# Kernel tuning notes

Measured on AMD Instinct MI355X. Metric: run time of the kernel, lower is better.

## Reference

```python
import jax, jax.numpy as jnp
import numpy as np

N = 100000
E = 1600000
C_IN = 128
C_OUT = 128
BN_EPS = 1e-5


def setup_inputs() -> dict:
    key = jax.random.key(0)
    k1, k2, k3, k4 = jax.random.split(key, 4)
    x = jax.random.normal(k1, (N, C_IN), dtype=jnp.float32)
    edge_index = jax.random.randint(k2, (2, E), 0, N, dtype=jnp.int64)
    edge_weight = jax.random.uniform(k3, (E,), dtype=jnp.float32)
    W = jax.random.normal(k4, (C_IN, C_OUT), dtype=jnp.float32) / np.sqrt(C_IN)
    gamma = jnp.ones((C_OUT,), dtype=jnp.float32)
    beta = jnp.zeros((C_OUT,), dtype=jnp.float32)
    return {"x": x, "edge_index": edge_index, "edge_weight": edge_weight,
            "W": W, "gamma": gamma, "beta": beta}


def reference(x, edge_index, edge_weight, W, gamma, beta):
    n = x.shape[0]
    row, col = edge_index[0], edge_index[1]  # messages flow row -> col
    loop = jnp.arange(n, dtype=edge_index.dtype)
    # GCNConv (improved=False): add self-loops with weight 1
    row_f = jnp.concatenate([row, loop])
    col_f = jnp.concatenate([col, loop])
    w_f = jnp.concatenate([edge_weight, jnp.ones((n,), x.dtype)])
    # symmetric normalization: D^{-1/2} A D^{-1/2}
    deg = jax.ops.segment_sum(w_f, col_f, num_segments=n)
    deg_safe = jnp.where(deg > 0, deg, 1.0)
    dis = jnp.where(deg > 0, jax.lax.rsqrt(deg_safe), 0.0)
    norm = dis[row_f] * w_f * dis[col_f]  # [E+N]
    # linear transform then scatter-add aggregation (bias=False)
    h = x @ W  # [N, C_out]
    agg = jax.ops.segment_sum(h[row_f] * norm[:, None], col_f, num_segments=n)
    # BatchNorm1d (training mode: batch stats, biased variance) + ReLU
    mean = agg.mean(axis=0)
    var = agg.var(axis=0)
    y = (agg - mean) * jax.lax.rsqrt(var + BN_EPS) * gamma + beta
    return jax.nn.relu(y)
```

## Files before the change

kernel.cpp:

```cpp
#include <hip/hip_runtime.h>

#define C 128
#define MAXNB 1024
typedef unsigned int uint;
typedef unsigned short ushort;
typedef __attribute__((ext_vector_type(4))) float f32x4;
typedef __attribute__((ext_vector_type(8))) short bf16x8;

__device__ __forceinline__ float blo(uint u) { return __uint_as_float(u << 16); }
__device__ __forceinline__ float bhi(uint u) { return __uint_as_float(u & 0xFFFF0000u); }
#define PACKBF(LO, HI) __builtin_amdgcn_perm(__float_as_uint(HI) + 0x8000u, \
                                             __float_as_uint(LO) + 0x8000u, 0x07060302u)

__global__ __launch_bounds__(256) void k_hist(const int* __restrict__ col,
                                              int* __restrict__ counts,
                                              int nE, int NB, int NBLK) {
    __shared__ int hist[MAXNB];
    const int t = threadIdx.x, blk = blockIdx.x;
    for (int i = t; i < NB; i += 256) hist[i] = 0;
    __syncthreads();
    const int base = blk * 2048;
    for (int k = 0; k < 8; ++k) {
        int e = base + k * 256 + t;
        if (e < nE) atomicAdd(&hist[col[e] >> 7], 1);
    }
    __syncthreads();
    for (int i = t; i < NB; i += 256) counts[i * NBLK + blk] = hist[i];
}

__global__ __launch_bounds__(256) void k_scan1(int* __restrict__ counts,
                                               int* __restrict__ bsum, int scanN) {
    __shared__ int s[256];
    int t = threadIdx.x;
    int i = blockIdx.x * 256 + t;
    int v = (i < scanN) ? counts[i] : 0;
    s[t] = v;
    __syncthreads();
    for (int d = 1; d < 256; d <<= 1) {
        int a = (t >= d) ? s[t - d] : 0;
        __syncthreads();
        s[t] += a;
        __syncthreads();
    }
    if (i < scanN) counts[i] = s[t] - v;
    if (t == 255) bsum[blockIdx.x] = s[255];
}

__global__ __launch_bounds__(256) void k_scan2(int* __restrict__ bsum, int nb) {
    __shared__ int s[256];
    __shared__ int carry;
    int t = threadIdx.x;
    if (t == 0) carry = 0;
    __syncthreads();
    int nch = (nb + 255) / 256;
    for (int c = 0; c < nch; ++c) {
        int i = c * 256 + t;
        int v = (i < nb) ? bsum[i] : 0;
        s[t] = v;
        __syncthreads();
        for (int d = 1; d < 256; d <<= 1) {
            int a = (t >= d) ? s[t - d] : 0;
            __syncthreads();
            s[t] += a;
            __syncthreads();
        }
        int cb = carry;
        if (i < nb) bsum[i] = s[t] - v + cb;
        int tot = s[255];
        __syncthreads();
        if (t == 0) carry = cb + tot;
        __syncthreads();
    }
}

__global__ __launch_bounds__(256) void k_scan3(int* __restrict__ counts,
                                               const int* __restrict__ bsum,
                                               int* __restrict__ bstart,
                                               int scanN, int NBLK, int NB, int nE) {
    int i = blockIdx.x * 256 + threadIdx.x;
    if (i >= scanN) return;
    int v = counts[i] + bsum[i >> 8];
    counts[i] = v;
    if (i % NBLK == 0) {
        bstart[i / NBLK] = v;
        if (i == 0) bstart[NB] = nE;
    }
}

__global__ __launch_bounds__(256) void k_scatter(const int* __restrict__ ei,
                                                 const float* __restrict__ ew,
                                                 const int* __restrict__ counts,
                                                 int2* __restrict__ ev2,
                                                 int nE, int NB, int NBLK) {
    __shared__ int base_l[MAXNB];
    __shared__ int cnt_l[MAXNB];
    const int t = threadIdx.x, blk = blockIdx.x;
    for (int i = t; i < NB; i += 256) {
        base_l[i] = counts[i * NBLK + blk];
        cnt_l[i] = 0;
    }
    __syncthreads();
    const int base = blk * 2048;
    for (int k = 0; k < 8; ++k) {
        int e = base + k * 256 + t;
        if (e >= nE) continue;
        int c = ei[nE + e];
        int row = ei[e];
        int b = c >> 7;
        int pos = base_l[b] + atomicAdd(&cnt_l[b], 1);
        ev2[pos] = make_int2(((c & 127) << 25) | row, __float_as_int(ew[e]));
    }
}

__global__ __launch_bounds__(256) void k_sortdeg(const int2* __restrict__ ev2,
                                                 const int* __restrict__ bstart,
                                                 int2* __restrict__ evs,
                                                 int* __restrict__ offs,
                                                 float* __restrict__ dis,
                                                 int n, int nE) {
    __shared__ int cnt[128];
    __shared__ float wsum[128];
    __shared__ int cur[128];
    __shared__ int sc[128];
    const int t = threadIdx.x, b = blockIdx.x;
    if (t < 128) { cnt[t] = 0; wsum[t] = 0.f; }
    __syncthreads();
    const int s = bstart[b], e = bstart[b + 1];
    for (int i = s + t; i < e; i += 256) {
        int2 E = ev2[i];
        int cl = (uint)E.x >> 25;
        atomicAdd(&cnt[cl], 1);
        atomicAdd(&wsum[cl], __int_as_float(E.y));
    }
    __syncthreads();
    if (t < 128) sc[t] = cnt[t];
    __syncthreads();
    for (int d = 1; d < 128; d <<= 1) {
        int v = 0;
        if (t < 128 && t >= d) v = sc[t - d];
        __syncthreads();
        if (t < 128) sc[t] += v;
        __syncthreads();
    }
    if (t < 128) {
        int col = (b << 7) + t;
        int base = s + sc[t] - cnt[t];
        cur[t] = base;
        if (col < n) {
            offs[col] = base;
            dis[col] = rsqrtf(1.0f + wsum[t]);
        }
    }
    if (b == 0 && t == 0) offs[n] = nE;
    __syncthreads();
    for (int i = s + t; i < e; i += 256) {
        int2 E = ev2[i];
        int cl = (uint)E.x >> 25;
        int pos = atomicAdd(&cur[cl], 1);
        evs[pos] = make_int2(E.x & 0x1FFFFFF, E.y);
    }
}

__global__ __launch_bounds__(256) void k_cvt(const float4* __restrict__ x4,
                                             const float* __restrict__ dis,
                                             ushort4* __restrict__ xb4, long total4) {
    long i = (long)blockIdx.x * 256 + threadIdx.x;
    if (i >= total4) return;
    float d = dis[i >> 5];
    float4 v = x4[i];
    ushort4 r;
#define RNE(OUT, F)                                                     \
    {                                                                   \
        uint u = __float_as_uint((F) * d);                              \
        OUT = (ushort)((u + 0x7FFFu + ((u >> 16) & 1u)) >> 16);         \
    }
    RNE(r.x, v.x) RNE(r.y, v.y) RNE(r.z, v.z) RNE(r.w, v.w)
#undef RNE
    xb4[i] = r;
}

__global__ __launch_bounds__(256) void k_wcvt(const float* __restrict__ W,
                                              ushort* __restrict__ WbT) {
    int idx = blockIdx.x * 256 + threadIdx.x;
    int k = idx >> 7, o = idx & 127;
    uint u = __float_as_uint(W[idx]);
    WbT[o * 128 + k] = (ushort)((u + 0x7FFFu + ((u >> 16) & 1u)) >> 16);
}

__global__ __launch_bounds__(256) void k_segagg(const ushort* __restrict__ xb,
                                                const int2* __restrict__ ev,
                                                const int* __restrict__ offs,
                                                const float* __restrict__ dis,
                                                ushort* __restrict__ aggb, int n) {
    const int lane = threadIdx.x & 15;
    const int sub  = threadIdx.x >> 4;
    const int col  = blockIdx.x * 16 + sub;
    if (col >= n) return;

    uint4 sv = *(const uint4*)(xb + (size_t)col * C + lane * 8);
    float acc[8] = {blo(sv.x), bhi(sv.x), blo(sv.y), bhi(sv.y),
                    blo(sv.z), bhi(sv.z), blo(sv.w), bhi(sv.w)};

    int i = offs[col];
    const int end = offs[col + 1];

#define EDGE(E, V)                                                        \
    {                                                                     \
        float nw = __int_as_float(E.y);                                   \
        acc[0] = fmaf(nw, blo(V.x), acc[0]);                              \
        acc[1] = fmaf(nw, bhi(V.x), acc[1]);                              \
        acc[2] = fmaf(nw, blo(V.y), acc[2]);                              \
        acc[3] = fmaf(nw, bhi(V.y), acc[3]);                              \
        acc[4] = fmaf(nw, blo(V.z), acc[4]);                              \
        acc[5] = fmaf(nw, bhi(V.z), acc[5]);                              \
        acc[6] = fmaf(nw, blo(V.w), acc[6]);                              \
        acc[7] = fmaf(nw, bhi(V.w), acc[7]);                              \
    }
#define GATH(K) uint4 v##K = *(const uint4*)(xb + (size_t)e##K.x * C + lane * 8);

    for (; i + 8 <= end; i += 8) {
        int2 e0 = ev[i],     e1 = ev[i + 1], e2 = ev[i + 2], e3 = ev[i + 3];
        int2 e4 = ev[i + 4], e5 = ev[i + 5], e6 = ev[i + 6], e7 = ev[i + 7];
        GATH(0) GATH(1) GATH(2) GATH(3) GATH(4) GATH(5) GATH(6) GATH(7)
        EDGE(e0, v0) EDGE(e1, v1) EDGE(e2, v2) EDGE(e3, v3)
        EDGE(e4, v4) EDGE(e5, v5) EDGE(e6, v6) EDGE(e7, v7)
    }
    for (; i + 2 <= end; i += 2) {
        int2 e0 = ev[i], e1 = ev[i + 1];
        GATH(0) GATH(1)
        EDGE(e0, v0) EDGE(e1, v1)
    }
    if (i < end) {
        int2 e0 = ev[i];
        GATH(0)
        EDGE(e0, v0)
    }
#undef GATH
#undef EDGE

    float d = dis[col];
    uint4 r;
    r.x = PACKBF(d * acc[0], d * acc[1]);
    r.y = PACKBF(d * acc[2], d * acc[3]);
    r.z = PACKBF(d * acc[4], d * acc[5]);
    r.w = PACKBF(d * acc[6], d * acc[7]);
    *(uint4*)(aggb + (size_t)col * C + lane * 8) = r;
}

__global__ __launch_bounds__(256, 4) void k_gemm(const ushort* __restrict__ aggb,
                                                 ushort* __restrict__ outb,
                                                 const ushort* __restrict__ WbT,
                                                 int n) {
    const int t = threadIdx.x;
    const int lane = t & 63;
    const int wv = t >> 6;
    const int lr = lane & 15;
    const int lk = lane >> 4;
    const long m = (long)blockIdx.x * 64 + wv * 16 + lr;
    const bool inr = m < (long)n;

    bf16x8 b0, b1, b2, b3;
    if (inr) {
        const bf16x8* p = (const bf16x8*)(aggb + (size_t)m * C + lk * 8);
        b0 = p[0];
        b1 = p[4];
        b2 = p[8];
        b3 = p[12];
    } else {
        b0 = b1 = b2 = b3 = (bf16x8){0, 0, 0, 0, 0, 0, 0, 0};
    }

    f32x4 acc[8];
#pragma unroll
    for (int ot = 0; ot < 8; ++ot) acc[ot] = (f32x4){0.f, 0.f, 0.f, 0.f};

#pragma unroll 2
    for (int ot = 0; ot < 8; ++ot) {
        const ushort* wp = WbT + (ot * 16 + lr) * 128 + lk * 8;
        bf16x8 a0 = *(const bf16x8*)(wp);
        bf16x8 a1 = *(const bf16x8*)(wp + 32);
        bf16x8 a2 = *(const bf16x8*)(wp + 64);
        bf16x8 a3 = *(const bf16x8*)(wp + 96);
        acc[ot] = __builtin_amdgcn_mfma_f32_16x16x32_bf16(a0, b0, acc[ot], 0, 0, 0);
        acc[ot] = __builtin_amdgcn_mfma_f32_16x16x32_bf16(a1, b1, acc[ot], 0, 0, 0);
        acc[ot] = __builtin_amdgcn_mfma_f32_16x16x32_bf16(a2, b2, acc[ot], 0, 0, 0);
        acc[ot] = __builtin_amdgcn_mfma_f32_16x16x32_bf16(a3, b3, acc[ot], 0, 0, 0);
    }

    if (inr) {
        ushort* orow = outb + (size_t)m * C + lk * 4;
#pragma unroll
        for (int ot = 0; ot < 8; ++ot) {
            uint2 r;
            r.x = PACKBF(acc[ot][0], acc[ot][1]);
            r.y = PACKBF(acc[ot][2], acc[ot][3]);
            *(uint2*)(orow + ot * 16) = r;
        }
    }
}

__global__ __launch_bounds__(1024) void k_stats(const uint4* __restrict__ ob4,
                                                float* __restrict__ part, int n) {
    const int t = threadIdx.x;
    const int cg = t & 15;
    const int rl = t >> 4;
    float s[8] = {0, 0, 0, 0, 0, 0, 0, 0};
    float q[8] = {0, 0, 0, 0, 0, 0, 0, 0};
    for (int r = blockIdx.x * 64 + rl; r < n; r += gridDim.x * 64) {
        uint4 v = ob4[(size_t)r * 16 + cg];
        float f0 = blo(v.x), f1 = bhi(v.x), f2 = blo(v.y), f3 = bhi(v.y);
        float f4 = blo(v.z), f5 = bhi(v.z), f6 = blo(v.w), f7 = bhi(v.w);
        s[0] += f0; q[0] = fmaf(f0, f0, q[0]);
        s[1] += f1; q[1] = fmaf(f1, f1, q[1]);
        s[2] += f2; q[2] = fmaf(f2, f2, q[2]);
        s[3] += f3; q[3] = fmaf(f3, f3, q[3]);
        s[4] += f4; q[4] = fmaf(f4, f4, q[4]);
        s[5] += f5; q[5] = fmaf(f5, f5, q[5]);
        s[6] += f6; q[6] = fmaf(f6, f6, q[6]);
        s[7] += f7; q[7] = fmaf(f7, f7, q[7]);
    }
#pragma unroll
    for (int j = 0; j < 8; ++j) {
        s[j] += __shfl_xor(s[j], 16); s[j] += __shfl_xor(s[j], 32);
        q[j] += __shfl_xor(q[j], 16); q[j] += __shfl_xor(q[j], 32);
    }
    __shared__ float lds_s[16][128];
    __shared__ float lds_q[16][128];
    const int wvi = t >> 6;
    if ((t & 63) < 16) {
#pragma unroll
        for (int j = 0; j < 8; ++j) {
            lds_s[wvi][cg * 8 + j] = s[j];
            lds_q[wvi][cg * 8 + j] = q[j];
        }
    }
    __syncthreads();
    if (t < 128) {
        float ps = 0.f;
#pragma unroll
        for (int w = 0; w < 16; ++w) ps += lds_s[w][t];
        part[(size_t)blockIdx.x * 256 + t] = ps;
    } else if (t < 256) {
        int c = t - 128;
        float pq = 0.f;
#pragma unroll
        for (int w = 0; w < 16; ++w) pq += lds_q[w][c];
        part[(size_t)blockIdx.x * 256 + t] = pq;
    }
}

__global__ __launch_bounds__(256) void k_finish(const float* __restrict__ part,
                                                float* __restrict__ sums, int nblk) {
    int t = threadIdx.x;
    float s = 0.f;
    for (int b = blockIdx.x; b < nblk; b += gridDim.x) s += part[(size_t)b * 256 + t];
    atomicAdd(&sums[t], s);
}

__global__ __launch_bounds__(256) void k_apply(const uint4* __restrict__ ob4,
                                               float* __restrict__ out,
                                               const float* __restrict__ sums,
                                               const float* __restrict__ gamma,
                                               const float* __restrict__ beta,
                                               int n) {
    size_t idx = (size_t)blockIdx.x * 256 + threadIdx.x;
    size_t total = (size_t)n * 16;
    if (idx >= total) return;
    int cg = (int)(idx & 15);
    int c0 = cg * 8;
    float inv_n = 1.0f / (float)n;
    uint4 v = ob4[idx];
    float f[8] = {blo(v.x), bhi(v.x), blo(v.y), bhi(v.y),
                  blo(v.z), bhi(v.z), blo(v.w), bhi(v.w)};
    float4 r0, r1;
#define BN1(OUT, J)                                                        \
    {                                                                      \
        float mean = sums[c0 + J] * inv_n;                                 \
        float var  = fmaxf(sums[C + c0 + J] * inv_n - mean * mean, 0.f);   \
        float sc   = rsqrtf(var + 1e-5f) * gamma[c0 + J];                  \
        OUT = fmaxf(fmaf(f[J] - mean, sc, beta[c0 + J]), 0.f);             \
    }
    BN1(r0.x, 0) BN1(r0.y, 1) BN1(r0.z, 2) BN1(r0.w, 3)
    BN1(r1.x, 4) BN1(r1.y, 5) BN1(r1.z, 6) BN1(r1.w, 7)
#undef BN1
    float4* orow = (float4*)(out + (idx >> 4) * C + c0);
    orow[0] = r0;
    orow[1] = r1;
}

extern "C" void kernel_launch(void* const* d_in, const int* in_sizes, int n_in,
                              void* d_out, int out_size, void* d_ws, size_t ws_size,
                              hipStream_t stream) {
    const float* x     = (const float*)d_in[0];
    const int*   ei    = (const int*)d_in[1];
    const float* ew    = (const float*)d_in[2];
    const float* W     = (const float*)d_in[3];
    const float* gamma = (const float*)d_in[4];
    const float* beta  = (const float*)d_in[5];

    const int n  = in_sizes[0] / C;
    const int nE = in_sizes[2];

    const int NB    = (n + 127) >> 7;
    const int NBLK  = (nE + 2047) / 2048;
    const int scanN = NB * NBLK;
    const int scanB = (scanN + 255) / 256;
    const int SB    = 256;

    float* out = (float*)d_out;
    char* p = (char*)d_ws;
#define ALLOC(TYPE, NAME, BYTES) \
    TYPE NAME = (TYPE)p; p += ((size_t)(BYTES) + 255) & ~(size_t)255;
    ALLOC(int2*,   ev2,    (size_t)nE * 8)
    ALLOC(int2*,   evs,    (size_t)nE * 8)
    ALLOC(ushort*, xb,     (size_t)n * C * 2)
    ALLOC(ushort*, aggb,   (size_t)n * C * 2)
    ALLOC(ushort*, outb,   (size_t)n * C * 2)
    ALLOC(int*,    counts, (size_t)scanN * 4)
    ALLOC(int*,    bsum,   (size_t)scanB * 4)
    ALLOC(int*,    bstart, (size_t)(NB + 1) * 4)
    ALLOC(float*,  dis,    (size_t)n * 4)
    ALLOC(int*,    offs,   (size_t)(n + 1) * 4)
    ALLOC(ushort*, WbT,    32768)
    ALLOC(float*,  sums,   1024)
    ALLOC(float*,  part,   (size_t)SB * 256 * 4)
#undef ALLOC

    const long total4 = (long)n * 32;
    const long totalb = (long)n * 16;

    hipMemsetAsync(sums, 0, 256 * 4, stream);

    k_hist   <<<NBLK, 256, 0, stream>>>(ei + nE, counts, nE, NB, NBLK);
    k_scan1  <<<scanB, 256, 0, stream>>>(counts, bsum, scanN);
    k_scan2  <<<1, 256, 0, stream>>>(bsum, scanB);
    k_scan3  <<<scanB, 256, 0, stream>>>(counts, bsum, bstart, scanN, NBLK, NB, nE);
    k_scatter<<<NBLK, 256, 0, stream>>>(ei, ew, counts, ev2, nE, NB, NBLK);
    k_sortdeg<<<NB, 256, 0, stream>>>(ev2, bstart, evs, offs, dis, n, nE);
    k_wcvt   <<<64, 256, 0, stream>>>(W, WbT);
    k_cvt    <<<(int)((total4 + 255) / 256), 256, 0, stream>>>((const float4*)x, dis, (ushort4*)xb, total4);
    k_segagg <<<(n + 15) / 16, 256, 0, stream>>>(xb, evs, offs, dis, aggb, n);
    k_gemm   <<<(n + 63) / 64, 256, 0, stream>>>(aggb, outb, WbT, n);
    k_stats  <<<SB, 1024, 0, stream>>>((const uint4*)outb, part, n);
    k_finish <<<16, 256, 0, stream>>>(part, sums, SB);
    k_apply  <<<(int)((totalb + 255) / 256), 256, 0, stream>>>((const uint4*)outb, out, sums, gamma, beta, n);
}
```

Before: 220.8 us.

## Process two destination nodes per thread group in segagg; enlarge hist/scatter blocks

The segment aggregation kernel now has each 16-lane group handle two destination nodes, interleaving their gathers so more independent loads are in flight. It also halves the grid. The histogram and scatter kernels move to 512-thread blocks covering 8192 edges each, which shrinks the count matrix and the scan work. The cost is fewer waves in segagg and more divergence when the two nodes have different degrees.

```diff
diff --git a/kernel.cpp b/kernel.cpp
--- a/kernel.cpp
+++ b/kernel.cpp
@@ -12,20 +12,20 @@
 #define PACKBF(LO, HI) __builtin_amdgcn_perm(__float_as_uint(HI) + 0x8000u, \
                                              __float_as_uint(LO) + 0x8000u, 0x07060302u)
 
-__global__ __launch_bounds__(256) void k_hist(const int* __restrict__ col,
+__global__ __launch_bounds__(512) void k_hist(const int* __restrict__ col,
                                               int* __restrict__ counts,
                                               int nE, int NB, int NBLK) {
     __shared__ int hist[MAXNB];
     const int t = threadIdx.x, blk = blockIdx.x;
-    for (int i = t; i < NB; i += 256) hist[i] = 0;
-    __syncthreads();
-    const int base = blk * 2048;
-    for (int k = 0; k < 8; ++k) {
-        int e = base + k * 256 + t;
+    for (int i = t; i < NB; i += 512) hist[i] = 0;
+    __syncthreads();
+    const int base = blk * 8192;
+    for (int k = 0; k < 16; ++k) {
+        int e = base + k * 512 + t;
         if (e < nE) atomicAdd(&hist[col[e] >> 7], 1);
     }
     __syncthreads();
-    for (int i = t; i < NB; i += 256) counts[i * NBLK + blk] = hist[i];
+    for (int i = t; i < NB; i += 512) counts[i * NBLK + blk] = hist[i];
 }
 
 __global__ __launch_bounds__(256) void k_scan1(int* __restrict__ counts,
@@ -87,7 +87,7 @@
     }
 }
 
-__global__ __launch_bounds__(256) void k_scatter(const int* __restrict__ ei,
+__global__ __launch_bounds__(512) void k_scatter(const int* __restrict__ ei,
                                                  const float* __restrict__ ew,
                                                  const int* __restrict__ counts,
                                                  int2* __restrict__ ev2,
@@ -95,14 +95,14 @@
     __shared__ int base_l[MAXNB];
     __shared__ int cnt_l[MAXNB];
     const int t = threadIdx.x, blk = blockIdx.x;
-    for (int i = t; i < NB; i += 256) {
+    for (int i = t; i < NB; i += 512) {
         base_l[i] = counts[i * NBLK + blk];
         cnt_l[i] = 0;
     }
     __syncthreads();
-    const int base = blk * 2048;
-    for (int k = 0; k < 8; ++k) {
-        int e = base + k * 256 + t;
+    const int base = blk * 8192;
+    for (int k = 0; k < 16; ++k) {
+        int e = base + k * 512 + t;
         if (e >= nE) continue;
         int c = ei[nE + e];
         int row = ei[e];
@@ -193,58 +193,94 @@
                                                 const float* __restrict__ dis,
                                                 ushort* __restrict__ aggb, int n) {
     const int lane = threadIdx.x & 15;
-    const int sub  = threadIdx.x >> 4;
-    const int col  = blockIdx.x * 16 + sub;
-    if (col >= n) return;
-
-    uint4 sv = *(const uint4*)(xb + (size_t)col * C + lane * 8);
-    float acc[8] = {blo(sv.x), bhi(sv.x), blo(sv.y), bhi(sv.y),
-                    blo(sv.z), bhi(sv.z), blo(sv.w), bhi(sv.w)};
-
-    int i = offs[col];
-    const int end = offs[col + 1];
-
-#define EDGE(E, V)                                                        \
+    const int g    = threadIdx.x >> 4;
+    const int colA = blockIdx.x * 32 + g * 2;
+    const int colB = colA + 1;
+    const bool vA = colA < n, vB = colB < n;
+
+    float accA[8] = {0.f, 0.f, 0.f, 0.f, 0.f, 0.f, 0.f, 0.f};
+    float accB[8] = {0.f, 0.f, 0.f, 0.f, 0.f, 0.f, 0.f, 0.f};
+    int iA = 0, eA = 0, iB = 0, eB = 0;
+
+    if (vA) {
+        uint4 sv = *(const uint4*)(xb + (size_t)colA * C + lane * 8);
+        accA[0] = blo(sv.x); accA[1] = bhi(sv.x); accA[2] = blo(sv.y); accA[3] = bhi(sv.y);
+        accA[4] = blo(sv.z); accA[5] = bhi(sv.z); accA[6] = blo(sv.w); accA[7] = bhi(sv.w);
+        iA = offs[colA]; eA = offs[colA + 1];
+    }
+    if (vB) {
+        uint4 sv = *(const uint4*)(xb + (size_t)colB * C + lane * 8);
+        accB[0] = blo(sv.x); accB[1] = bhi(sv.x); accB[2] = blo(sv.y); accB[3] = bhi(sv.y);
+        accB[4] = blo(sv.z); accB[5] = bhi(sv.z); accB[6] = blo(sv.w); accB[7] = bhi(sv.w);
+        iB = offs[colB]; eB = offs[colB + 1];
+    }
+
+#define EDGE(ACC, E, V)                                                   \
     {                                                                     \
         float nw = __int_as_float(E.y);                                   \
-        acc[0] = fmaf(nw, blo(V.x), acc[0]);                              \
-        acc[1] = fmaf(nw, bhi(V.x), acc[1]);                              \
-        acc[2] = fmaf(nw, blo(V.y), acc[2]);                              \
-        acc[3] = fmaf(nw, bhi(V.y), acc[3]);                              \
-        acc[4] = fmaf(nw, blo(V.z), acc[4]);                              \
-        acc[5] = fmaf(nw, bhi(V.z), acc[5]);                              \
-        acc[6] = fmaf(nw, blo(V.w), acc[6]);                              \
-        acc[7] = fmaf(nw, bhi(V.w), acc[7]);                              \
-    }
-#define GATH(K) uint4 v##K = *(const uint4*)(xb + (size_t)e##K.x * C + lane * 8);
-
-    for (; i + 8 <= end; i += 8) {
-        int2 e0 = ev[i],     e1 = ev[i + 1], e2 = ev[i + 2], e3 = ev[i + 3];
-        int2 e4 = ev[i + 4], e5 = ev[i + 5], e6 = ev[i + 6], e7 = ev[i + 7];
-        GATH(0) GATH(1) GATH(2) GATH(3) GATH(4) GATH(5) GATH(6) GATH(7)
-        EDGE(e0, v0) EDGE(e1, v1) EDGE(e2, v2) EDGE(e3, v3)
-        EDGE(e4, v4) EDGE(e5, v5) EDGE(e6, v6) EDGE(e7, v7)
-    }
-    for (; i + 2 <= end; i += 2) {
-        int2 e0 = ev[i], e1 = ev[i + 1];
-        GATH(0) GATH(1)
-        EDGE(e0, v0) EDGE(e1, v1)
-    }
-    if (i < end) {
-        int2 e0 = ev[i];
-        GATH(0)
-        EDGE(e0, v0)
+        ACC[0] = fmaf(nw, blo(V.x), ACC[0]);                              \
+        ACC[1] = fmaf(nw, bhi(V.x), ACC[1]);                              \
+        ACC[2] = fmaf(nw, blo(V.y), ACC[2]);                              \
+        ACC[3] = fmaf(nw, bhi(V.y), ACC[3]);                              \
+        ACC[4] = fmaf(nw, blo(V.z), ACC[4]);                              \
+        ACC[5] = fmaf(nw, bhi(V.z), ACC[5]);                              \
+        ACC[6] = fmaf(nw, blo(V.w), ACC[6]);                              \
+        ACC[7] = fmaf(nw, bhi(V.w), ACC[7]);                              \
+    }
+#define GATH(V, E) uint4 V = *(const uint4*)(xb + (size_t)(E).x * C + lane * 8);
+
+    while (iA + 4 <= eA && iB + 4 <= eB) {
+        int2 a0 = ev[iA], a1 = ev[iA + 1], a2 = ev[iA + 2], a3 = ev[iA + 3];
+        int2 b0 = ev[iB], b1 = ev[iB + 1], b2 = ev[iB + 2], b3 = ev[iB + 3];
+        GATH(va0, a0) GATH(vb0, b0) GATH(va1, a1) GATH(vb1, b1)
+        GATH(va2, a2) GATH(vb2, b2) GATH(va3, a3) GATH(vb3, b3)
+        EDGE(accA, a0, va0) EDGE(accB, b0, vb0)
+        EDGE(accA, a1, va1) EDGE(accB, b1, vb1)
+        EDGE(accA, a2, va2) EDGE(accB, b2, vb2)
+        EDGE(accA, a3, va3) EDGE(accB, b3, vb3)
+        iA += 4; iB += 4;
+    }
+    for (; iA + 4 <= eA; iA += 4) {
+        int2 a0 = ev[iA], a1 = ev[iA + 1], a2 = ev[iA + 2], a3 = ev[iA + 3];
+        GATH(v0, a0) GATH(v1, a1) GATH(v2, a2) GATH(v3, a3)
+        EDGE(accA, a0, v0) EDGE(accA, a1, v1) EDGE(accA, a2, v2) EDGE(accA, a3, v3)
+    }
+    for (; iA < eA; ++iA) {
+        int2 a0 = ev[iA];
+        GATH(v0, a0)
+        EDGE(accA, a0, v0)
+    }
+    for (; iB + 4 <= eB; iB += 4) {
+        int2 b0 = ev[iB], b1 = ev[iB + 1], b2 = ev[iB + 2], b3 = ev[iB + 3];
+        GATH(v0, b0) GATH(v1, b1) GATH(v2, b2) GATH(v3, b3)
+        EDGE(accB, b0, v0) EDGE(accB, b1, v1) EDGE(accB, b2, v2) EDGE(accB, b3, v3)
+    }
+    for (; iB < eB; ++iB) {
+        int2 b0 = ev[iB];
+        GATH(v0, b0)
+        EDGE(accB, b0, v0)
     }
 #undef GATH
 #undef EDGE
 
-    float d = dis[col];
-    uint4 r;
-    r.x = PACKBF(d * acc[0], d * acc[1]);
-    r.y = PACKBF(d * acc[2], d * acc[3]);
-    r.z = PACKBF(d * acc[4], d * acc[5]);
-    r.w = PACKBF(d * acc[6], d * acc[7]);
-    *(uint4*)(aggb + (size_t)col * C + lane * 8) = r;
+    if (vA) {
+        float d = dis[colA];
+        uint4 r;
+        r.x = PACKBF(d * accA[0], d * accA[1]);
+        r.y = PACKBF(d * accA[2], d * accA[3]);
+        r.z = PACKBF(d * accA[4], d * accA[5]);
+        r.w = PACKBF(d * accA[6], d * accA[7]);
+        *(uint4*)(aggb + (size_t)colA * C + lane * 8) = r;
+    }
+    if (vB) {
+        float d = dis[colB];
+        uint4 r;
+        r.x = PACKBF(d * accB[0], d * accB[1]);
+        r.y = PACKBF(d * accB[2], d * accB[3]);
+        r.z = PACKBF(d * accB[4], d * accB[5]);
+        r.w = PACKBF(d * accB[6], d * accB[7]);
+        *(uint4*)(aggb + (size_t)colB * C + lane * 8) = r;
+    }
 }
 
 __global__ __launch_bounds__(256, 4) void k_gemm(const ushort* __restrict__ aggb,
@@ -402,7 +438,7 @@
     const int nE = in_sizes[2];
 
     const int NB    = (n + 127) >> 7;
-    const int NBLK  = (nE + 2047) / 2048;
+    const int NBLK  = (nE + 8191) / 8192;
     const int scanN = NB * NBLK;
     const int scanB = (scanN + 255) / 256;
     const int SB    = 256;
@@ -431,15 +467,15 @@
 
     hipMemsetAsync(sums, 0, 256 * 4, stream);
 
-    k_hist   <<<NBLK, 256, 0, stream>>>(ei + nE, counts, nE, NB, NBLK);
+    k_hist   <<<NBLK, 512, 0, stream>>>(ei + nE, counts, nE, NB, NBLK);
     k_scan1  <<<scanB, 256, 0, stream>>>(counts, bsum, scanN);
     k_scan2  <<<1, 256, 0, stream>>>(bsum, scanB);
     k_scan3  <<<scanB, 256, 0, stream>>>(counts, bsum, bstart, scanN, NBLK, NB, nE);
-    k_scatter<<<NBLK, 256, 0, stream>>>(ei, ew, counts, ev2, nE, NB, NBLK);
+    k_scatter<<<NBLK, 512, 0, stream>>>(ei, ew, counts, ev2, nE, NB, NBLK);
     k_sortdeg<<<NB, 256, 0, stream>>>(ev2, bstart, evs, offs, dis, n, nE);
     k_wcvt   <<<64, 256, 0, stream>>>(W, WbT);
     k_cvt    <<<(int)((total4 + 255) / 256), 256, 0, stream>>>((const float4*)x, dis, (ushort4*)xb, total4);
-    k_segagg <<<(n + 15) / 16, 256, 0, stream>>>(xb, evs, offs, dis, aggb, n);
+    k_segagg <<<(n + 31) / 32, 256, 0, stream>>>(xb, evs, offs, dis, aggb, n);
     k_gemm   <<<(n + 63) / 64, 256, 0, stream>>>(aggb, outb, WbT, n);
     k_stats  <<<SB, 1024, 0, stream>>>((const uint4*)outb, part, n);
     k_finish <<<16, 256, 0, stream>>>(part, sums, SB);
```

After: 211.5 us. 1.04x faster.

## Enlarge histogram blocks, fold scan3 into consumers, merge W conversion into cvt

Applied to the files above, without the earlier changes.

Histogram and scatter blocks now process 8192 edges with 512 threads, which cuts the counts matrix and scan work about fourfold. The k_scan3 kernel is removed: scatter and sortdeg add the block-sum carry themselves when reading counts, and the bstart array goes away. The W transpose/convert work runs as extra blocks of the x-convert kernel, so there are two fewer launches. The trade-off is fewer blocks, and so less parallelism, in the hist and scatter kernels.

```diff
diff --git a/kernel.cpp b/kernel.cpp
--- a/kernel.cpp
+++ b/kernel.cpp
@@ -12,20 +12,20 @@
 #define PACKBF(LO, HI) __builtin_amdgcn_perm(__float_as_uint(HI) + 0x8000u, \
                                              __float_as_uint(LO) + 0x8000u, 0x07060302u)
 
-__global__ __launch_bounds__(256) void k_hist(const int* __restrict__ col,
+__global__ __launch_bounds__(512) void k_hist(const int* __restrict__ col,
                                               int* __restrict__ counts,
                                               int nE, int NB, int NBLK) {
     __shared__ int hist[MAXNB];
     const int t = threadIdx.x, blk = blockIdx.x;
-    for (int i = t; i < NB; i += 256) hist[i] = 0;
-    __syncthreads();
-    const int base = blk * 2048;
-    for (int k = 0; k < 8; ++k) {
-        int e = base + k * 256 + t;
+    for (int i = t; i < NB; i += 512) hist[i] = 0;
+    __syncthreads();
+    const int base = blk * 8192;
+    for (int k = 0; k < 16; ++k) {
+        int e = base + k * 512 + t;
         if (e < nE) atomicAdd(&hist[col[e] >> 7], 1);
     }
     __syncthreads();
-    for (int i = t; i < NB; i += 256) counts[i * NBLK + blk] = hist[i];
+    for (int i = t; i < NB; i += 512) counts[i * NBLK + blk] = hist[i];
 }
 
 __global__ __launch_bounds__(256) void k_scan1(int* __restrict__ counts,
@@ -73,36 +73,24 @@
     }
 }
 
-__global__ __launch_bounds__(256) void k_scan3(int* __restrict__ counts,
-                                               const int* __restrict__ bsum,
-                                               int* __restrict__ bstart,
-                                               int scanN, int NBLK, int NB, int nE) {
-    int i = blockIdx.x * 256 + threadIdx.x;
-    if (i >= scanN) return;
-    int v = counts[i] + bsum[i >> 8];
-    counts[i] = v;
-    if (i % NBLK == 0) {
-        bstart[i / NBLK] = v;
-        if (i == 0) bstart[NB] = nE;
-    }
-}
-
-__global__ __launch_bounds__(256) void k_scatter(const int* __restrict__ ei,
+__global__ __launch_bounds__(512) void k_scatter(const int* __restrict__ ei,
                                                  const float* __restrict__ ew,
                                                  const int* __restrict__ counts,
+                                                 const int* __restrict__ bsum,
                                                  int2* __restrict__ ev2,
                                                  int nE, int NB, int NBLK) {
     __shared__ int base_l[MAXNB];
     __shared__ int cnt_l[MAXNB];
     const int t = threadIdx.x, blk = blockIdx.x;
-    for (int i = t; i < NB; i += 256) {
-        base_l[i] = counts[i * NBLK + blk];
+    for (int i = t; i < NB; i += 512) {
+        int idx = i * NBLK + blk;
+        base_l[i] = counts[idx] + bsum[idx >> 8];
         cnt_l[i] = 0;
     }
     __syncthreads();
-    const int base = blk * 2048;
-    for (int k = 0; k < 8; ++k) {
-        int e = base + k * 256 + t;
+    const int base = blk * 8192;
+    for (int k = 0; k < 16; ++k) {
+        int e = base + k * 512 + t;
         if (e >= nE) continue;
         int c = ei[nE + e];
         int row = ei[e];
@@ -113,19 +101,28 @@
 }
 
 __global__ __launch_bounds__(256) void k_sortdeg(const int2* __restrict__ ev2,
-                                                 const int* __restrict__ bstart,
+                                                 const int* __restrict__ counts,
+                                                 const int* __restrict__ bsum,
                                                  int2* __restrict__ evs,
                                                  int* __restrict__ offs,
                                                  float* __restrict__ dis,
-                                                 int n, int nE) {
+                                                 int n, int nE, int NB, int NBLK) {
     __shared__ int cnt[128];
     __shared__ float wsum[128];
     __shared__ int cur[128];
     __shared__ int sc[128];
+    __shared__ int seg[2];
     const int t = threadIdx.x, b = blockIdx.x;
     if (t < 128) { cnt[t] = 0; wsum[t] = 0.f; }
-    __syncthreads();
-    const int s = bstart[b], e = bstart[b + 1];
+    if (t == 0) {
+        int i0 = b * NBLK;
+        seg[0] = counts[i0] + bsum[i0 >> 8];
+    } else if (t == 1) {
+        int i1 = (b + 1) * NBLK;
+        seg[1] = (b + 1 < NB) ? counts[i1] + bsum[i1 >> 8] : nE;
+    }
+    __syncthreads();
+    const int s = seg[0], e = seg[1];
     for (int i = s + t; i < e; i += 256) {
         int2 E = ev2[i];
         int cl = (uint)E.x >> 25;
@@ -163,7 +160,17 @@
 
 __global__ __launch_bounds__(256) void k_cvt(const float4* __restrict__ x4,
                                              const float* __restrict__ dis,
-                                             ushort4* __restrict__ xb4, long total4) {
+                                             ushort4* __restrict__ xb4,
+                                             const float* __restrict__ W,
+                                             ushort* __restrict__ WbT,
+                                             long total4, int cvtB) {
+    if ((int)blockIdx.x >= cvtB) {
+        int idx = ((int)blockIdx.x - cvtB) * 256 + threadIdx.x;
+        int k = idx >> 7, o = idx & 127;
+        uint u = __float_as_uint(W[idx]);
+        WbT[o * 128 + k] = (ushort)((u + 0x7FFFu + ((u >> 16) & 1u)) >> 16);
+        return;
+    }
     long i = (long)blockIdx.x * 256 + threadIdx.x;
     if (i >= total4) return;
     float d = dis[i >> 5];
@@ -177,14 +184,6 @@
     RNE(r.x, v.x) RNE(r.y, v.y) RNE(r.z, v.z) RNE(r.w, v.w)
 #undef RNE
     xb4[i] = r;
-}
-
-__global__ __launch_bounds__(256) void k_wcvt(const float* __restrict__ W,
-                                              ushort* __restrict__ WbT) {
-    int idx = blockIdx.x * 256 + threadIdx.x;
-    int k = idx >> 7, o = idx & 127;
-    uint u = __float_as_uint(W[idx]);
-    WbT[o * 128 + k] = (ushort)((u + 0x7FFFu + ((u >> 16) & 1u)) >> 16);
 }
 
 __global__ __launch_bounds__(256) void k_segagg(const ushort* __restrict__ xb,
@@ -402,7 +401,7 @@
     const int nE = in_sizes[2];
 
     const int NB    = (n + 127) >> 7;
-    const int NBLK  = (nE + 2047) / 2048;
+    const int NBLK  = (nE + 8191) / 8192;
     const int scanN = NB * NBLK;
     const int scanB = (scanN + 255) / 256;
     const int SB    = 256;
@@ -418,7 +417,6 @@
     ALLOC(ushort*, outb,   (size_t)n * C * 2)
     ALLOC(int*,    counts, (size_t)scanN * 4)
     ALLOC(int*,    bsum,   (size_t)scanB * 4)
-    ALLOC(int*,    bstart, (size_t)(NB + 1) * 4)
     ALLOC(float*,  dis,    (size_t)n * 4)
     ALLOC(int*,    offs,   (size_t)(n + 1) * 4)
     ALLOC(ushort*, WbT,    32768)
@@ -428,17 +426,16 @@
 
     const long total4 = (long)n * 32;
     const long totalb = (long)n * 16;
+    const int  cvtB   = (int)((total4 + 255) / 256);
 
     hipMemsetAsync(sums, 0, 256 * 4, stream);
 
-    k_hist   <<<NBLK, 256, 0, stream>>>(ei + nE, counts, nE, NB, NBLK);
+    k_hist   <<<NBLK, 512, 0, stream>>>(ei + nE, counts, nE, NB, NBLK);
     k_scan1  <<<scanB, 256, 0, stream>>>(counts, bsum, scanN);
     k_scan2  <<<1, 256, 0, stream>>>(bsum, scanB);
-    k_scan3  <<<scanB, 256, 0, stream>>>(counts, bsum, bstart, scanN, NBLK, NB, nE);
-    k_scatter<<<NBLK, 256, 0, stream>>>(ei, ew, counts, ev2, nE, NB, NBLK);
-    k_sortdeg<<<NB, 256, 0, stream>>>(ev2, bstart, evs, offs, dis, n, nE);
-    k_wcvt   <<<64, 256, 0, stream>>>(W, WbT);
-    k_cvt    <<<(int)((total4 + 255) / 256), 256, 0, stream>>>((const float4*)x, dis, (ushort4*)xb, total4);
+    k_scatter<<<NBLK, 512, 0, stream>>>(ei, ew, counts, bsum, ev2, nE, NB, NBLK);
+    k_sortdeg<<<NB, 256, 0, stream>>>(ev2, counts, bsum, evs, offs, dis, n, nE, NB, NBLK);
+    k_cvt    <<<cvtB + 64, 256, 0, stream>>>((const float4*)x, dis, (ushort4*)xb, W, WbT, total4, cvtB);
     k_segagg <<<(n + 15) / 16, 256, 0, stream>>>(xb, evs, offs, dis, aggb, n);
     k_gemm   <<<(n + 63) / 64, 256, 0, stream>>>(aggb, outb, WbT, n);
     k_stats  <<<SB, 1024, 0, stream>>>((const uint4*)outb, part, n);
```

Measured after the change: 198.9 us. 10.0% less time.
